# Kernel optimization log

Hardware: AMD Instinct MI355X
Metric: run time of the kernel (lower is better)

## Reference

```python
import jax, jax.numpy as jnp
import numpy as np

# FP4 (E2M1) format constants from the source module
EXP_BITS = 2
MANT_BITS = 1
EXP_BIAS = 1          # 2**(EXP_BITS-1) - 1
FP4_MAX = 6.0         # (1 + 1/2) * 2**( (2**EXP_BITS - 1) - EXP_BIAS )
GROUP = 128           # w_group_size


def _float_to_fp4(x):
    """Encode float -> 4-bit code (sign|exp|mant) with subnormal support.
    Mirrors _float_to_fp(x, exp_bits=2, mant_bits=1, exp_bias=1)."""
    sign = (x < 0).astype(jnp.int32)
    xa = jnp.abs(x)
    zero = xa == 0
    xs = jnp.where(zero, jnp.float32(1e-8), xa)
    max_exp_field = (1 << EXP_BITS) - 1           # 3
    min_normal_exp = 1 - EXP_BIAS                 # 0
    exp_val = jnp.floor(jnp.log2(xs)).astype(jnp.int32)
    is_sub = exp_val < min_normal_exp
    exp_clamped = jnp.clip(exp_val, min_normal_exp, max_exp_field - EXP_BIAS)
    exp_unbiased = exp_clamped + EXP_BIAS
    ms = 1 << MANT_BITS                           # 2
    mant_normal = jnp.clip(
        jnp.round((xs / jnp.exp2(exp_clamped.astype(jnp.float32)) - 1.0) * ms),
        0, ms - 1).astype(jnp.int32)
    mant_sub = jnp.clip(
        jnp.round(xs / jnp.float32(2.0 ** min_normal_exp) * ms),
        0, ms - 1).astype(jnp.int32)
    exp_field = jnp.where(is_sub, 0, exp_unbiased)
    mant_field = jnp.where(is_sub, mant_sub, mant_normal)
    code = (sign << (EXP_BITS + MANT_BITS)) | (exp_field << MANT_BITS) | mant_field
    return jnp.where(zero, 0, code)


def _fp4_to_float(code):
    """Decode 4-bit code -> float32, with subnormals. Mirrors _fp_to_float."""
    zero = code == 0
    sign = ((code >> (EXP_BITS + MANT_BITS)) & 1).astype(jnp.float32)
    raw_exp = ((code >> MANT_BITS) & ((1 << EXP_BITS) - 1)).astype(jnp.float32)
    mant = (code & ((1 << MANT_BITS) - 1)).astype(jnp.float32)
    value_normal = (1.0 + mant / float(1 << MANT_BITS)) * jnp.exp2(raw_exp - EXP_BIAS)
    value_sub = mant / float(1 << MANT_BITS) * jnp.exp2(jnp.float32(1 - EXP_BIAS))
    v = jnp.where(raw_exp == 0, value_sub, value_normal)
    v = jnp.where(sign == 1, -v, v)
    return jnp.where(zero, jnp.float32(0.0), v)


def quantize_dequantize_weight(w):
    """Group-wise (group=128 along in_features) fp4 quantize-dequantize."""
    O, I = w.shape
    wg = w.reshape(O, I // GROUP, GROUP)
    scale = jnp.max(jnp.abs(wg), axis=-1, keepdims=True) / FP4_MAX
    scale = jnp.maximum(scale, jnp.float32(1e-8))
    code = _float_to_fp4(wg / scale)            # int32 codes in [0, 15]
    deq = _fp4_to_float(code) * scale
    return deq.reshape(O, I)


def setup_inputs() -> dict:
    key = jax.random.key(0)
    k1, k2, k3 = jax.random.split(key, 3)
    x = jax.random.normal(k1, (4, 2048, 4096), dtype=jnp.float32)
    weight = jax.random.normal(k2, (4096, 4096), dtype=jnp.float32) * 0.02
    bias = jax.random.normal(k3, (4096,), dtype=jnp.float32) * 0.01
    return {"x": x, "weight": weight, "bias": bias}


def reference(x, weight, bias):
    # fake-quantize weights to FP4 (E2M1) group-wise, then F.linear
    w_deq = quantize_dequantize_weight(weight)
    return jnp.einsum('bsi,oi->bso', x, w_deq) + bias
```

## Files before the change

kernel.cpp:

```cpp
#include <hip/hip_runtime.h>
#include <stdint.h>

#define M_TOT 8192
#define N_TOT 4096
#define K_TOT 4096
#define NTILE 64

typedef __attribute__((ext_vector_type(8))) short bf16x8;
typedef __attribute__((ext_vector_type(4))) float f32x4;
typedef __attribute__((ext_vector_type(2))) unsigned short u16x2;
typedef __attribute__((ext_vector_type(4))) unsigned short u16x4;

typedef const __attribute__((address_space(1))) void* gas1;
typedef __attribute__((address_space(3))) void* las3;

__device__ __forceinline__ unsigned short bf16_rne(float f) {
    union { float f; unsigned int u; } v; v.f = f;
    unsigned int u = v.u;
    return (unsigned short)((u + 0x7FFFu + ((u >> 16) & 1u)) >> 16);
}

__device__ __forceinline__ float fp4_qdq(float wv, float scale) {
    float a = fabsf(wv) / scale;
    float q;
    if      (a <= 0.25f) q = 0.0f;
    else if (a <  1.0f ) q = 0.5f;
    else if (a <= 1.25f) q = 1.0f;
    else if (a <  2.0f ) q = 1.5f;
    else if (a <= 2.5f ) q = 2.0f;
    else if (a <  4.0f ) q = 3.0f;
    else if (a <= 5.0f ) q = 4.0f;
    else                 q = 6.0f;
    float d = q * scale;
    return wv < 0.0f ? -d : d;
}

__global__ __launch_bounds__(256) void prep_kernel(const float* __restrict__ w,
                                                   unsigned short* __restrict__ wb,
                                                   const float* __restrict__ x,
                                                   unsigned short* __restrict__ xb) {
    if (blockIdx.x < 2048) {
        const int total4 = (M_TOT * K_TOT) / 4;
        int stride = 2048 * 256;
        for (int i = blockIdx.x * 256 + threadIdx.x; i < total4; i += stride) {
            float4 v = ((const float4*)x)[i];
            u16x4 o;
            o.x = bf16_rne(v.x); o.y = bf16_rne(v.y);
            o.z = bf16_rne(v.z); o.w = bf16_rne(v.w);
            ((u16x4*)xb)[i] = o;
        }
    } else {
        int wv0 = (blockIdx.x - 2048) * 4 + (threadIdx.x >> 6);
        int lane = threadIdx.x & 63;
        const int ngroups = (N_TOT * K_TOT) / 128;
        for (int g = wv0; g < ngroups; g += 2048 * 4) {
            size_t base = (size_t)g * 128;
            float2 v = ((const float2*)(w + base))[lane];
            float mx = fmaxf(fabsf(v.x), fabsf(v.y));
            #pragma unroll
            for (int off = 32; off; off >>= 1) mx = fmaxf(mx, __shfl_xor(mx, off));
            float scale = fmaxf(mx / 6.0f, 1e-8f);
            u16x2 o;
            o.x = bf16_rne(fp4_qdq(v.x, scale));
            o.y = bf16_rne(fp4_qdq(v.y, scale));
            *(u16x2*)(wb + base + (size_t)lane * 2) = o;
        }
    }
}


#define BAR()      __builtin_amdgcn_s_barrier()
#define SCHEDB()   __builtin_amdgcn_sched_barrier(0)
#define WAITVM6()  asm volatile("s_waitcnt vmcnt(6)" ::: "memory")
#define WAITVM0()  asm volatile("s_waitcnt vmcnt(0)" ::: "memory")

__global__ __launch_bounds__(512) void gemm_kernel(const unsigned short* __restrict__ A,
                                                   const unsigned short* __restrict__ B,
                                                   const float* __restrict__ bias,
                                                   float* __restrict__ C) {
    extern __shared__ unsigned char lds[];

    const int bid = blockIdx.x;
    const int xcd = bid & 7;
    const int idx = bid >> 3;
    const int tm = ((xcd >> 2) << 4) + (idx >> 2);
    const int tn = ((xcd & 3) << 2) + (idx & 3);
    const int m0 = tm << 8, n0 = tn << 8;

    const int t = threadIdx.x;
    const int l = t & 63;
    const int wid = t >> 6;
    const int wr = wid >> 2;
    const int wc = wid & 3;
    const int l15 = l & 15;
    const int q4 = l >> 4;

    unsigned offA[8];
    #pragma unroll
    for (int QM = 0; QM < 2; ++QM)
        #pragma unroll
        for (int i = 0; i < 4; ++i) {
            int ra = wr * 128 + QM * 64 + i * 16 + l15;
            unsigned pa = (unsigned)((q4 + (ra >> 1)) & 3);
            offA[QM * 4 + i] = (unsigned)ra * 64u + pa * 16u;
        }
    unsigned offB[4];
    #pragma unroll
    for (int n = 0; n < 4; ++n) {
        int rb = wc * 64 + n * 16 + l15;
        unsigned pb = (unsigned)((q4 + (rb >> 1)) & 3);
        offB[n] = 65536u + (unsigned)rb * 64u + pb * 16u;
    }

    const int r0g = t >> 2,        p0g = t & 3;
    const int r1g = (512 + t) >> 2, p1g = t & 3;
    const int s0g = (p0g - (r0g >> 1)) & 3;
    const int s1g = (p1g - (r1g >> 1)) & 3;
    const unsigned short* arow0 = A + (size_t)(m0 + r0g) * K_TOT + s0g * 8;
    const unsigned short* arow1 = A + (size_t)(m0 + r1g) * K_TOT + s1g * 8;
    const unsigned short* brow0 = B + (size_t)(n0 + r0g) * K_TOT + s0g * 8;
    const unsigned short* brow1 = B + (size_t)(n0 + r1g) * K_TOT + s1g * 8;
    const unsigned lo0 = (unsigned)t * 16u;
    const unsigned lo1 = lo0 + 8192u;

#define STAGE(ROW0, ROW1, MATOFF, KK, TT, BB) do {                                   \
      const unsigned _base = (MATOFF) + (unsigned)(BB) * 32768u + (KK) * 16384u;     \
      const int _ko = (TT) * 64 + (KK) * 32;                                         \
      __builtin_amdgcn_global_load_lds((gas1)(ROW0 + _ko), (las3)(lds + _base + lo0), 16, 0, 0); \
      __builtin_amdgcn_global_load_lds((gas1)(ROW1 + _ko), (las3)(lds + _base + lo1), 16, 0, 0); \
    } while (0)
#define STAGE_A(KK, TT, BB) STAGE(arow0, arow1, 0u, KK, TT, BB)
#define STAGE_B(KK, TT, BB) STAGE(brow0, brow1, 65536u, KK, TT, BB)

#define LOAD_A(QM, KK, BB) do {                                                      \
      _Pragma("unroll")                                                              \
      for (int i = 0; i < 4; ++i)                                                    \
        af[i] = *(const bf16x8*)(lds + ((BB) * 32768u + (KK) * 16384u)               \
                                 + offA[(QM) * 4 + i]);                              \
    } while (0)

#define LOAD_B(KK, BB) do {                                                          \
      _Pragma("unroll")                                                              \
      for (int n = 0; n < 4; ++n)                                                    \
        bg[n] = *(const bf16x8*)(lds + ((BB) * 32768u + (KK) * 16384u) + offB[n]);   \
    } while (0)

#define MFMA16(QM) do {                                                              \
      _Pragma("unroll")                                                              \
      for (int i = 0; i < 4; ++i)                                                    \
        _Pragma("unroll")                                                            \
        for (int n = 0; n < 4; ++n)                                                  \
          acc[(QM) * 4 + i][n] = __builtin_amdgcn_mfma_f32_16x16x32_bf16(            \
              af[i], bg[n], acc[(QM) * 4 + i][n], 0, 0, 0);                          \
    } while (0)

#define KTILE(U, BB) do {                                                            \
      const int tt1 = ((U) + 1 < NTILE) ? (U) + 1 : (U) - 1;                         \
      const int tt2 = ((U) + 2 < NTILE) ? (U) + 2 : (U);                             \
                                                             \
      LOAD_B(0, BB); LOAD_A(0, 0, BB);                                               \
      STAGE_A(1, tt1, 1 - (BB));                                                     \
      BAR();                                                                         \
      __builtin_amdgcn_s_setprio(1); MFMA16(0); __builtin_amdgcn_s_setprio(0);       \
      BAR();                                                                         \
                                                             \
      LOAD_A(1, 0, BB);                                                              \
      STAGE_B(0, tt2, BB);                                                           \
      BAR();                                                                         \
      __builtin_amdgcn_s_setprio(1); MFMA16(1); __builtin_amdgcn_s_setprio(0);       \
      BAR();                                                                         \
                                                             \
      LOAD_B(1, BB); LOAD_A(0, 1, BB);                                               \
      STAGE_A(0, tt2, BB);                                                           \
      BAR();                                                                         \
      __builtin_amdgcn_s_setprio(1); MFMA16(0); __builtin_amdgcn_s_setprio(0);       \
      BAR();                                                                         \
                                                             \
      LOAD_A(1, 1, BB);                                                              \
      STAGE_B(1, tt2, BB);                                                           \
      BAR();                                                                         \
      __builtin_amdgcn_s_setprio(1); MFMA16(1); __builtin_amdgcn_s_setprio(0);       \
      WAITVM6(); SCHEDB(); BAR();                                                    \
    } while (0)

    f32x4 acc[8][4];
    #pragma unroll
    for (int i = 0; i < 8; ++i)
        #pragma unroll
        for (int j = 0; j < 4; ++j)
            acc[i][j] = (f32x4)0.0f;
    bf16x8 af[4], bg[4];

    STAGE_A(0, 0, 0); STAGE_B(0, 0, 0); STAGE_A(1, 0, 0); STAGE_B(1, 0, 0);
    STAGE_A(0, 1, 1); STAGE_B(0, 1, 1); STAGE_B(1, 1, 1);
    WAITVM6(); SCHEDB();
    BAR();

    #pragma unroll 1
    for (int u = 0; u < NTILE; u += 2) {
        KTILE(u, 0);
        KTILE(u + 1, 1);
    }
    WAITVM0();

    #pragma unroll
    for (int j = 0; j < 4; ++j) {
        int n = n0 + wc * 64 + j * 16 + l15;
        float bv = bias[n];
        #pragma unroll
        for (int i = 0; i < 8; ++i) {
            int mb = m0 + wr * 128 + i * 16 + (q4 << 2);
            #pragma unroll
            for (int r = 0; r < 4; ++r)
                C[(size_t)(mb + r) * N_TOT + n] = acc[i][j][r] + bv;
        }
    }
}

extern "C" void kernel_launch(void* const* d_in, const int* in_sizes, int n_in,
                              void* d_out, int out_size, void* d_ws, size_t ws_size,
                              hipStream_t stream) {
    const float* x    = (const float*)d_in[0];
    const float* w    = (const float*)d_in[1];
    const float* bias = (const float*)d_in[2];
    float* out = (float*)d_out;

    unsigned short* wb = (unsigned short*)d_ws;
    unsigned short* xb = wb + (size_t)N_TOT * K_TOT;

    prep_kernel<<<4096, 256, 0, stream>>>(w, wb, x, xb);

    hipFuncSetAttribute(reinterpret_cast<const void*>(gemm_kernel),
                        hipFuncAttributeMaxDynamicSharedMemorySize, 131072);
    gemm_kernel<<<512, 512, 131072, stream>>>(xb, wb, bias, out);
}
```

Baseline: 288.8 us.

## Restructure GEMM k-tile into two phases with 32 MFMAs per barrier

Each k-tile now runs as two phases instead of four. Each phase loads both A halves and B fragments from LDS, issues the global-to-LDS stages for both A and B, then runs 32 MFMAs between barriers. This halves the barrier count per tile and gives the MFMA bursts longer to hide loads. The cost is a larger A fragment register array (8 instead of 4), a different prefetch schedule with a vmcnt(8) wait, and possibly higher register pressure under the 512-thread launch bound.

```diff
diff --git a/kernel.cpp b/kernel.cpp
--- a/kernel.cpp
+++ b/kernel.cpp
@@ -71,7 +71,7 @@
 
 #define BAR()      __builtin_amdgcn_s_barrier()
 #define SCHEDB()   __builtin_amdgcn_sched_barrier(0)
-#define WAITVM6()  asm volatile("s_waitcnt vmcnt(6)" ::: "memory")
+#define WAITVM8()  asm volatile("s_waitcnt vmcnt(8)" ::: "memory")
 #define WAITVM0()  asm volatile("s_waitcnt vmcnt(0)" ::: "memory")
 
 __global__ __launch_bounds__(512) void gemm_kernel(const unsigned short* __restrict__ A,
@@ -135,8 +135,8 @@
 #define LOAD_A(QM, KK, BB) do {                                                      \
       _Pragma("unroll")                                                              \
       for (int i = 0; i < 4; ++i)                                                    \
-        af[i] = *(const bf16x8*)(lds + ((BB) * 32768u + (KK) * 16384u)               \
-                                 + offA[(QM) * 4 + i]);                              \
+        af[(QM) * 4 + i] = *(const bf16x8*)(lds + ((BB) * 32768u + (KK) * 16384u)    \
+                                            + offA[(QM) * 4 + i]);                   \
     } while (0)
 
 #define LOAD_B(KK, BB) do {                                                          \
@@ -151,36 +151,26 @@
         _Pragma("unroll")                                                            \
         for (int n = 0; n < 4; ++n)                                                  \
           acc[(QM) * 4 + i][n] = __builtin_amdgcn_mfma_f32_16x16x32_bf16(            \
-              af[i], bg[n], acc[(QM) * 4 + i][n], 0, 0, 0);                          \
+              af[(QM) * 4 + i], bg[n], acc[(QM) * 4 + i][n], 0, 0, 0);               \
     } while (0)
 
 #define KTILE(U, BB) do {                                                            \
       const int tt1 = ((U) + 1 < NTILE) ? (U) + 1 : (U) - 1;                         \
       const int tt2 = ((U) + 2 < NTILE) ? (U) + 2 : (U);                             \
-                                                             \
-      LOAD_B(0, BB); LOAD_A(0, 0, BB);                                               \
-      STAGE_A(1, tt1, 1 - (BB));                                                     \
+                                                               \
+      LOAD_B(0, BB); LOAD_A(0, 0, BB); LOAD_A(1, 0, BB);                             \
+      STAGE_A(1, tt1, 1 - (BB)); STAGE_B(1, tt1, 1 - (BB));                          \
       BAR();                                                                         \
-      __builtin_amdgcn_s_setprio(1); MFMA16(0); __builtin_amdgcn_s_setprio(0);       \
+      __builtin_amdgcn_s_setprio(1); MFMA16(0); MFMA16(1);                           \
+      __builtin_amdgcn_s_setprio(0);                                                 \
+      WAITVM8(); SCHEDB(); BAR();                                                    \
+                                                               \
+      LOAD_B(1, BB); LOAD_A(0, 1, BB); LOAD_A(1, 1, BB);                             \
+      STAGE_A(0, tt2, BB); STAGE_B(0, tt2, BB);                                      \
       BAR();                                                                         \
-                                                             \
-      LOAD_A(1, 0, BB);                                                              \
-      STAGE_B(0, tt2, BB);                                                           \
-      BAR();                                                                         \
-      __builtin_amdgcn_s_setprio(1); MFMA16(1); __builtin_amdgcn_s_setprio(0);       \
-      BAR();                                                                         \
-                                                             \
-      LOAD_B(1, BB); LOAD_A(0, 1, BB);                                               \
-      STAGE_A(0, tt2, BB);                                                           \
-      BAR();                                                                         \
-      __builtin_amdgcn_s_setprio(1); MFMA16(0); __builtin_amdgcn_s_setprio(0);       \
-      BAR();                                                                         \
-                                                             \
-      LOAD_A(1, 1, BB);                                                              \
-      STAGE_B(1, tt2, BB);                                                           \
-      BAR();                                                                         \
-      __builtin_amdgcn_s_setprio(1); MFMA16(1); __builtin_amdgcn_s_setprio(0);       \
-      WAITVM6(); SCHEDB(); BAR();                                                    \
+      __builtin_amdgcn_s_setprio(1); MFMA16(0); MFMA16(1);                           \
+      __builtin_amdgcn_s_setprio(0);                                                 \
+      WAITVM8(); SCHEDB(); BAR();                                                    \
     } while (0)
 
     f32x4 acc[8][4];
@@ -189,11 +179,11 @@
         #pragma unroll
         for (int j = 0; j < 4; ++j)
             acc[i][j] = (f32x4)0.0f;
-    bf16x8 af[4], bg[4];
+    bf16x8 af[8], bg[4];
 
     STAGE_A(0, 0, 0); STAGE_B(0, 0, 0); STAGE_A(1, 0, 0); STAGE_B(1, 0, 0);
-    STAGE_A(0, 1, 1); STAGE_B(0, 1, 1); STAGE_B(1, 1, 1);
-    WAITVM6(); SCHEDB();
+    STAGE_A(0, 1, 1); STAGE_B(0, 1, 1);
+    WAITVM8(); SCHEDB();
     BAR();
 
     #pragma unroll 1
```

Result: no change. 293.8 us (+1.7%).
